# Optimization experiments

Hardware: AMD Instinct MI355X
Metric: run time of the kernel (lower is better)

Reference implementation:

```python
import jax, jax.numpy as jnp
import numpy as np
import math

Re = 0.15
DX = 1.0
UB = -1.0
NZ, NY, NX = 64, 256, 256
DT = 0.5
ITERATION = 2

def conv3(x, w, stride=1):
    return jax.lax.conv_general_dilated(x, w, (stride, stride, stride), 'VALID', dimension_numbers=('NCDHW', 'OIDHW', 'NCDHW'))

def pad1(x):
    return jnp.pad(x, ((0, 0), (0, 0), (1, 1), (1, 1), (1, 1)))

def bc_u(u):
    p = pad1(u)
    p = p.at[0, 0, :, :, 0].set(UB)
    p = p.at[0, 0, :, :, -1].set(UB)
    p = p.at[0, 0, :, 0, :].set(p[0, 0, :, 1, :])
    p = p.at[0, 0, :, -1, :].set(p[0, 0, :, -2, :])
    p = p.at[0, 0, 0, :, :].set(0.0)
    p = p.at[0, 0, -1, :, :].set(p[0, 0, -2, :, :])
    return p

def bc_v(v):
    # x faces, y faces, z-bottom are zero -> already satisfied by zero padding
    p = pad1(v)
    p = p.at[0, 0, -1, :, :].set(p[0, 0, -2, :, :])
    return p

def bc_w(w):
    # all six faces zero
    return pad1(w)

def bc_p(q):
    p = pad1(q)
    p = p.at[0, 0, :, :, 0].set(p[0, 0, :, :, 1])
    p = p.at[0, 0, :, :, -1].set(0.0)
    p = p.at[0, 0, :, 0, :].set(p[0, 0, :, 1, :])
    p = p.at[0, 0, :, -1, :].set(p[0, 0, :, -2, :])
    p = p.at[0, 0, 0, :, :].set(p[0, 0, 1, :, :])
    p = p.at[0, 0, -1, :, :].set(p[0, 0, -2, :, :])
    return p

def solid_body(u, v, w, sigma, dt):
    s = 1.0 / (1.0 + dt * sigma)
    return u * s, v * s, w * s

def prol(x):
    # nearest-neighbour upsample x2 in z, y, x
    return jnp.repeat(jnp.repeat(jnp.repeat(x, 2, axis=2), 2, axis=3), 2, axis=4)

def all_ads(uu, vv, ww, w1, w2, w3, w4):
    return (conv3(uu, w2), conv3(uu, w3), conv3(uu, w4),
            conv3(vv, w2), conv3(vv, w3), conv3(vv, w4),
            conv3(ww, w2), conv3(ww, w3), conv3(ww, w4),
            conv3(uu, w1), conv3(vv, w1), conv3(ww, w1))

def pg_vector(uu, vv, ww, u, v, w, k1, sigma, dt, w_diff, ads):
    ADx_u, ADy_u, ADz_u, ADx_v, ADy_v, ADz_v, ADx_w, ADy_w, ADz_w, AD2_u, AD2_v, AD2_w = ads
    speed = jnp.abs(u) * DX + jnp.abs(v) * DX + jnp.abs(w) * DX
    c = DX ** -3
    def kd(AD2, ax, ay, az):
        num = 0.1 * DX * jnp.abs((1.0 / 3.0) * c * speed * AD2)
        den = 0.001 + (jnp.abs(ax) * c + jnp.abs(ay) * c + jnp.abs(az) * c) / 3.0
        return num / den
    inv = 1.0 / (1.0 + dt * sigma)
    k_u = jnp.minimum(kd(AD2_u, ADx_u, ADy_u, ADz_u), k1) * inv
    k_v = jnp.minimum(kd(AD2_v, ADx_v, ADy_v, ADz_v), k1) * inv
    k_w = jnp.minimum(kd(AD2_w, ADx_w, ADy_w, ADz_w), k1) * inv
    # boundary_condition_k zeroes every halo face -> plain zero pad
    kuu, kvv, kww = pad1(k_u), pad1(k_v), pad1(k_w)
    k_x = 0.5 * (k_u * AD2_u + conv3(uu * kuu, w_diff) - u * conv3(kuu, w_diff))
    k_y = 0.5 * (k_v * AD2_v + conv3(vv * kvv, w_diff) - v * conv3(kvv, w_diff))
    k_z = 0.5 * (k_w * AD2_w + conv3(ww * kww, w_diff) - w * conv3(kww, w_diff))
    return k_x, k_y, k_z

def f_cycle_mg(uu, vv, ww, p, wA, w2, w3, w4, w_res, iteration, diag, dt, nlevel, ratio_x, ratio_y):
    b = -(conv3(uu, w2) + conv3(vv, w3) + conv3(ww, w4)) / dt
    w = jnp.zeros((1, 1, 2, 2 * ratio_y, 2 * ratio_x), b.dtype)
    r = b
    for _ in range(iteration):
        w = jnp.zeros((1, 1, 2, 2 * ratio_y, 2 * ratio_x), b.dtype)
        r = conv3(bc_p(p), wA) - b
        r_s = [r]
        for _ in range(1, nlevel - 1):
            r = conv3(r, w_res, stride=2)
            r_s.append(r)
        for i in reversed(range(1, nlevel - 1)):
            # boundary_condition_cw zeroes every halo face -> plain zero pad
            w = w - conv3(pad1(w), wA) / diag + r_s[i] / diag
            w = prol(w)
        p = p - w
        p = p - conv3(bc_p(p), wA) / diag + b / diag
    return p, w, r

def forward(values_u, values_v, values_w, values_p, k1, sigma, wA, w1, w2, w3, w4, w_res, dt, iteration):
    nz, ny, nx = values_u.shape[2], values_u.shape[3], values_u.shape[4]
    nlevel = int(math.log2(min(nx, ny, nz))) + 1
    ratio_x, ratio_y = nx // nz, ny // nz
    diag = wA[0, 0, 1, 1, 1]
    u, v, w = solid_body(values_u, values_v, values_w, sigma, dt)
    uu, vv, ww = bc_u(u), bc_v(v), bc_w(w)
    pp = bc_p(values_p)
    Gpx, Gpy, Gpz = conv3(pp, w2) * dt, conv3(pp, w3) * dt, conv3(pp, w4) * dt
    ads = all_ads(uu, vv, ww, w1, w2, w3, w4)
    k_x, k_y, k_z = pg_vector(uu, vv, ww, u, v, w, k1, sigma, dt, w1, ads)
    ADx_u, ADy_u, ADz_u, ADx_v, ADy_v, ADz_v, ADx_w, ADy_w, ADz_w, AD2_u, AD2_v, AD2_w = ads
    # predictor half step
    b_u = u + 0.5 * (Re * AD2_u * dt - u * ADx_u * dt - v * ADy_u * dt - w * ADz_u * dt) + 0.5 * k_x * dt - Gpx
    b_v = v + 0.5 * (Re * AD2_v * dt - u * ADx_v * dt - v * ADy_v * dt - w * ADz_v * dt) + 0.5 * k_y * dt - Gpy
    b_w = w + 0.5 * (Re * AD2_w * dt - u * ADx_w * dt - v * ADy_w * dt - w * ADz_w * dt) + 0.5 * k_z * dt - Gpz
    b_u, b_v, b_w = solid_body(b_u, b_v, b_w, sigma, dt)
    buu, bvv, bww = bc_u(b_u), bc_v(b_v), bc_w(b_w)
    ads = all_ads(buu, bvv, bww, w1, w2, w3, w4)
    k_x, k_y, k_z = pg_vector(buu, bvv, bww, b_u, b_v, b_w, k1, sigma, dt, w1, ads)
    ADx_u, ADy_u, ADz_u, ADx_v, ADy_v, ADz_v, ADx_w, ADy_w, ADz_w, AD2_u, AD2_v, AD2_w = ads
    # corrector full step
    u = u + Re * AD2_u * dt - b_u * ADx_u * dt - b_v * ADy_u * dt - b_w * ADz_u * dt + k_x * dt - Gpx
    v = v + Re * AD2_v * dt - b_u * ADx_v * dt - b_v * ADy_v * dt - b_w * ADz_v * dt + k_y * dt - Gpy
    w = w + Re * AD2_w * dt - b_u * ADx_w * dt - b_v * ADy_w * dt - b_w * ADz_w * dt + k_z * dt - Gpz
    u, v, w = solid_body(u, v, w, sigma, dt)
    uu, vv, ww = bc_u(u), bc_v(v), bc_w(w)
    p, w_mg, r = f_cycle_mg(uu, vv, ww, values_p, wA, w2, w3, w4, w_res, iteration, diag, dt, nlevel, ratio_x, ratio_y)
    # pressure-gradient velocity correction
    pp = bc_p(p)
    u = u - conv3(pp, w2) * dt
    v = v - conv3(pp, w3) * dt
    w = w - conv3(pp, w4) * dt
    u, v, w = solid_body(u, v, w, sigma, dt)
    return u, v, w, p, w_mg, r

def setup_inputs():
    key = jax.random.key(0)
    ks = jax.random.split(key, 4)
    f32 = jnp.float32
    shp = (1, 1, NZ, NY, NX)
    pshp = (1, 1, NZ + 2, NY + 2, NX + 2)
    lap = np.full((3, 3, 3), 1.0 / 26.0, np.float32)
    lap[1, 1, 1] = -1.0
    wA = jnp.asarray(lap.reshape(1, 1, 3, 3, 3))
    w1 = wA / (DX * DX)
    def cdiff(axis):
        k = np.zeros((3, 3, 3), np.float32)
        idx = [1, 1, 1]
        idx[axis] = 0
        k[tuple(idx)] = -0.5
        idx[axis] = 2
        k[tuple(idx)] = 0.5
        return jnp.asarray(k.reshape(1, 1, 3, 3, 3))
    w4, w3, w2 = cdiff(0), cdiff(1), cdiff(2)  # z, y, x advection stencils
    w_res = jnp.full((1, 1, 2, 2, 2), 0.125, f32)
    return dict(
        values_u=0.1 * jax.random.normal(ks[0], shp, f32),
        values_uu=jnp.zeros(pshp, f32),
        values_v=0.1 * jax.random.normal(ks[1], shp, f32),
        values_vv=jnp.zeros(pshp, f32),
        values_w=0.1 * jax.random.normal(ks[2], shp, f32),
        values_ww=jnp.zeros(pshp, f32),
        values_p=0.1 * jax.random.normal(ks[3], shp, f32),
        values_pp=jnp.zeros(pshp, f32),
        b_uu=jnp.zeros(pshp, f32), b_vv=jnp.zeros(pshp, f32), b_ww=jnp.zeros(pshp, f32),
        k1=2.0 * jnp.ones(shp, f32),
        k_uu=jnp.zeros(pshp, f32), k_vv=jnp.zeros(pshp, f32), k_ww=jnp.zeros(pshp, f32),
        sigma=jnp.zeros(shp, f32),
        wA=wA, w1=w1, w2=w2, w3=w3, w4=w4, w_res=w_res,
        dt=DT, iteration=ITERATION,
    )

def reference(values_u, values_uu, values_v, values_vv, values_w, values_ww, values_p, values_pp, b_uu, b_vv, b_ww, k1, k_uu, k_vv, k_ww, sigma, wA, w1, w2, w3, w4, w_res, dt, iteration):
    # padded scratch buffers (values_uu, ..., k_ww) are fully overwritten by the
    # boundary-condition routines, so the functional version rebuilds them via padding
    return forward(values_u, values_v, values_w, values_p, k1, sigma, wA, w1, w2, w3, w4, w_res, dt, iteration)
```

## Files before the change

kernel.cpp:

```cpp
#include <hip/hip_runtime.h>


#define RE_  0.15f
#define UB_  (-1.0f)
#define NZc  64
#define NYc  256
#define NXc  256
#define PZc  (NZc + 2)
#define PYc  (NYc + 2)
#define PXc  (NXc + 2)
#define Ncell  (NZc * NYc * NXc)
#define PNcell (PZc * PYc * PXc)

#define TBX 32
#define TBY 8
#define TZS 16

__device__ __forceinline__ int PIDX(int z, int y, int x) { return (z * PYc + y) * PXc + x; }
__device__ __forceinline__ int IDX (int z, int y, int x) { return (z * NYc + y) * NXc + x; }


struct PS {
  float s, c, xm, xp, ym, yp;
};
__device__ __forceinline__ PS rdp(const float* __restrict__ b, int pz, int iy, int ix) {
  PS q; q.s = 0.f;
#pragma unroll
  for (int dy = 0; dy < 3; ++dy) {
    int base = PIDX(pz, iy + dy, ix);
#pragma unroll
    for (int dx = 0; dx < 3; ++dx) {
      float v = b[base + dx];
      q.s += v;
      if (dy == 1 && dx == 1) q.c  = v;
      if (dy == 1 && dx == 0) q.xm = v;
      if (dy == 1 && dx == 2) q.xp = v;
      if (dy == 0 && dx == 1) q.ym = v;
      if (dy == 2 && dx == 1) q.yp = v;
    }
  }
  return q;
}

struct PS2 {
  float sv, svk, sk, vc, vxm, vxp, vym, vyp, kc;
};
__device__ __forceinline__ PS2 rdp2(const float* __restrict__ V, const float* __restrict__ K,
                                    int pz, int iy, int ix) {
  PS2 q; q.sv = 0.f; q.svk = 0.f; q.sk = 0.f;
#pragma unroll
  for (int dy = 0; dy < 3; ++dy) {
    int base = PIDX(pz, iy + dy, ix);
#pragma unroll
    for (int dx = 0; dx < 3; ++dx) {
      float v = V[base + dx], k = K[base + dx];
      q.sv += v; q.svk += v * k; q.sk += k;
      if (dy == 1 && dx == 1) { q.vc = v; q.kc = k; }
      if (dy == 1 && dx == 0) q.vxm = v;
      if (dy == 1 && dx == 2) q.vxp = v;
      if (dy == 0 && dx == 1) q.vym = v;
      if (dy == 2 && dx == 1) q.vyp = v;
    }
  }
  return q;
}

struct PR { float s, c; };
__device__ __forceinline__ PR rdpr(const float* __restrict__ b, int pz, int iy, int ix) {
  PR q; q.s = 0.f;
#pragma unroll
  for (int dy = 0; dy < 3; ++dy) {
    int base = PIDX(pz, iy + dy, ix);
#pragma unroll
    for (int dx = 0; dx < 3; ++dx) {
      float v = b[base + dx];
      q.s += v;
      if (dy == 1 && dx == 1) q.c = v;
    }
  }
  return q;
}


__global__ void k_scale_interior(const float* __restrict__ u0, const float* __restrict__ v0,
                                 const float* __restrict__ w0, const float* __restrict__ sigma,
                                 const float* __restrict__ dtp,
                                 float* __restrict__ Au, float* __restrict__ Av, float* __restrict__ Aw) {
  int i = blockIdx.x * blockDim.x + threadIdx.x;
  if (i >= Ncell) return;
  int x = i % NXc; int t = i / NXc; int y = t % NYc; int z = t / NYc;
  float s = 1.0f / (1.0f + dtp[0] * sigma[i]);
  int pi = PIDX(z + 1, y + 1, x + 1);
  Au[pi] = u0[i] * s;
  Av[pi] = v0[i] * s;
  Aw[pi] = w0[i] * s;
}

__global__ void k_halo_uvw(float* __restrict__ Au, float* __restrict__ Av, float* __restrict__ Aw) {
  int i = blockIdx.x * blockDim.x + threadIdx.x;
  if (i >= PNcell) return;
  int x = i % PXc; int t = i / PXc; int y = t % PYc; int z = t / PYc;
  if (z >= 1 && z <= NZc && y >= 1 && y <= NYc && x >= 1 && x <= NXc) return;
  float vu;
  if (z == 0) {
    vu = 0.0f;
  } else {
    int zz = (z == PZc - 1) ? NZc : z;
    if (x == 0 || x == PXc - 1) {
      vu = UB_;
    } else {
      int yy = y < 1 ? 1 : (y > NYc ? NYc : y);
      vu = Au[PIDX(zz, yy, x)];
    }
  }
  Au[i] = vu;
  float vv;
  if (z == 0 || x == 0 || x == PXc - 1 || y == 0 || y == PYc - 1) {
    vv = 0.0f;
  } else {
    vv = Av[PIDX(NZc, y, x)];
  }
  Av[i] = vv;
  Aw[i] = 0.0f;
}

__global__ void k_pad_p_interior(const float* __restrict__ p, float* __restrict__ pp) {
  int i = blockIdx.x * blockDim.x + threadIdx.x;
  if (i >= Ncell) return;
  int x = i % NXc; int t = i / NXc; int y = t % NYc; int z = t / NYc;
  pp[PIDX(z + 1, y + 1, x + 1)] = p[i];
}

__global__ void k_halo_p(float* __restrict__ pp) {
  int i = blockIdx.x * blockDim.x + threadIdx.x;
  if (i >= PNcell) return;
  int x = i % PXc; int t = i / PXc; int y = t % PYc; int z = t / PYc;
  if (z >= 1 && z <= NZc && y >= 1 && y <= NYc && x >= 1 && x <= NXc) return;
  float v;
  if (x == PXc - 1) {
    v = 0.0f;
  } else {
    int zz = z < 1 ? 1 : (z > NZc ? NZc : z);
    int yy = y < 1 ? 1 : (y > NYc ? NYc : y);
    int xx = (x == 0) ? 1 : x;
    v = pp[PIDX(zz, yy, xx)];
  }
  pp[i] = v;
}

__global__ void k_zero_halo3(float* __restrict__ a, float* __restrict__ b, float* __restrict__ c) {
  int i = blockIdx.x * blockDim.x + threadIdx.x;
  if (i >= PNcell) return;
  int x = i % PXc; int t = i / PXc; int y = t % PYc; int z = t / PYc;
  if (z >= 1 && z <= NZc && y >= 1 && y <= NYc && x >= 1 && x <= NXc) return;
  a[i] = 0.f; b[i] = 0.f; c[i] = 0.f;
}

__global__ void k_grad_p(const float* __restrict__ pp, const float* __restrict__ wx,
                         const float* __restrict__ wy, const float* __restrict__ wz,
                         const float* __restrict__ dtp,
                         float* __restrict__ gx, float* __restrict__ gy, float* __restrict__ gz) {
  int i = blockIdx.x * blockDim.x + threadIdx.x;
  if (i >= Ncell) return;
  int x = i % NXc; int t = i / NXc; int y = t % NYc; int z = t / NYc;
  float dt = dtp[0];
  gx[i] = (wx[12] * pp[PIDX(z + 1, y + 1, x)] + wx[14] * pp[PIDX(z + 1, y + 1, x + 2)]) * dt;
  gy[i] = (wy[10] * pp[PIDX(z + 1, y, x + 1)] + wy[16] * pp[PIDX(z + 1, y + 2, x + 1)]) * dt;
  gz[i] = (wz[4] * pp[PIDX(z, y + 1, x + 1)] + wz[22] * pp[PIDX(z + 2, y + 1, x + 1)]) * dt;
}

__global__ void k_div(const float* __restrict__ Au, const float* __restrict__ Av,
                      const float* __restrict__ Aw, const float* __restrict__ wx,
                      const float* __restrict__ wy, const float* __restrict__ wz,
                      const float* __restrict__ dtp, float* __restrict__ b) {
  int i = blockIdx.x * blockDim.x + threadIdx.x;
  if (i >= Ncell) return;
  int x = i % NXc; int t = i / NXc; int y = t % NYc; int z = t / NYc;
  float dx = wx[12] * Au[PIDX(z + 1, y + 1, x)] + wx[14] * Au[PIDX(z + 1, y + 1, x + 2)];
  float dy = wy[10] * Av[PIDX(z + 1, y, x + 1)] + wy[16] * Av[PIDX(z + 1, y + 2, x + 1)];
  float dz = wz[4] * Aw[PIDX(z, y + 1, x + 1)] + wz[22] * Aw[PIDX(z + 2, y + 1, x + 1)];
  b[i] = -(dx + dy + dz) / dtp[0];
}

__global__ void k_copy(const float* __restrict__ s, float* __restrict__ d, int n) {
  int i = blockIdx.x * blockDim.x + threadIdx.x;
  if (i < n) d[i] = s[i];
}

__global__ void k_restrict(const float* __restrict__ in, float* __restrict__ out,
                           int onz, int ony, int onx, const float* __restrict__ wres) {
  int i = blockIdx.x * blockDim.x + threadIdx.x;
  int tot = onz * ony * onx;
  if (i >= tot) return;
  int X = i % onx; int t = i / onx; int Y = t % ony; int Z = t / ony;
  int iny = ony * 2, inx = onx * 2;
  float s = 0.f;
#pragma unroll
  for (int dz = 0; dz < 2; ++dz)
#pragma unroll
    for (int dy = 0; dy < 2; ++dy)
#pragma unroll
      for (int dx = 0; dx < 2; ++dx)
        s += wres[(dz * 2 + dy) * 2 + dx] * in[((2 * Z + dz) * iny + 2 * Y + dy) * inx + 2 * X + dx];
  out[i] = s;
}

__global__ void k_up(const float* __restrict__ win, const float* __restrict__ r,
                     float* __restrict__ wout, int nz, int ny, int nx,
                     const float* __restrict__ wA, int first) {
  int i = blockIdx.x * blockDim.x + threadIdx.x;
  int tot = nz * ny * nx;
  if (i >= tot) return;
  int X = i % nx; int t = i / nx; int Y = t % ny; int Z = t / ny;
  float diag = wA[13];
  float val;
  if (first) {
    val = r[i] / diag;
  } else {
    float lap = 0.f;
#pragma unroll
    for (int dz = 0; dz < 3; ++dz)
#pragma unroll
      for (int dy = 0; dy < 3; ++dy)
#pragma unroll
        for (int dx = 0; dx < 3; ++dx) {
          int zz = Z + dz - 1, yy = Y + dy - 1, xx = X + dx - 1;
          if (zz >= 0 && zz < nz && yy >= 0 && yy < ny && xx >= 0 && xx < nx)
            lap += wA[(dz * 3 + dy) * 3 + dx] * win[(zz * ny + yy) * nx + xx];
        }
    val = win[i] - lap / diag + r[i] / diag;
  }
  int ony = 2 * ny, onx = 2 * nx;
#pragma unroll
  for (int dz = 0; dz < 2; ++dz)
#pragma unroll
    for (int dy = 0; dy < 2; ++dy)
#pragma unroll
      for (int dx = 0; dx < 2; ++dx)
        wout[((2 * Z + dz) * ony + (2 * Y + dy)) * onx + (2 * X + dx)] = val;
}

__global__ void k_sub_f(float* __restrict__ p, const float* __restrict__ w0,
                        float* __restrict__ pp) {
  int i = blockIdx.x * blockDim.x + threadIdx.x;
  if (i >= Ncell) return;
  int x = i % NXc; int t = i / NXc; int y = t % NYc; int z = t / NYc;
  float v = p[i] - w0[i];
  p[i] = v;
  pp[PIDX(z + 1, y + 1, x + 1)] = v;
}

__global__ void k_final(const float* __restrict__ Au, const float* __restrict__ Av,
                        const float* __restrict__ Aw, const float* __restrict__ pp,
                        const float* __restrict__ wx, const float* __restrict__ wy,
                        const float* __restrict__ wz, const float* __restrict__ sigma,
                        const float* __restrict__ dtp,
                        float* __restrict__ ou, float* __restrict__ ov, float* __restrict__ ow) {
  int i = blockIdx.x * blockDim.x + threadIdx.x;
  if (i >= Ncell) return;
  int x = i % NXc; int t = i / NXc; int y = t % NYc; int z = t / NYc;
  float dt = dtp[0];
  float inv = 1.0f / (1.0f + dt * sigma[i]);
  int pc = PIDX(z + 1, y + 1, x + 1);
  float dx = wx[12] * pp[PIDX(z + 1, y + 1, x)] + wx[14] * pp[PIDX(z + 1, y + 1, x + 2)];
  float dy = wy[10] * pp[PIDX(z + 1, y, x + 1)] + wy[16] * pp[PIDX(z + 1, y + 2, x + 1)];
  float dz = wz[4] * pp[PIDX(z, y + 1, x + 1)] + wz[22] * pp[PIDX(z + 2, y + 1, x + 1)];
  ou[i] = (Au[pc] - dx * dt) * inv;
  ov[i] = (Av[pc] - dy * dt) * inv;
  ow[i] = (Aw[pc] - dz * dt) * inv;
}


__global__ __launch_bounds__(256) void k_compute_k_t(
    const float* __restrict__ Au, const float* __restrict__ Av, const float* __restrict__ Aw,
    const float* __restrict__ k1, const float* __restrict__ sigma, const float* __restrict__ dtp,
    const float* __restrict__ w1, const float* __restrict__ wx, const float* __restrict__ wy,
    const float* __restrict__ wz,
    float* __restrict__ Ku, float* __restrict__ Kv, float* __restrict__ Kw) {
  int ix = blockIdx.x * TBX + threadIdx.x;
  int iy = blockIdx.y * TBY + threadIdx.y;
  int z0 = blockIdx.z * TZS;
  float dt = dtp[0];
  float wo = w1[0], wcd = w1[13] - wo;
  float cxm = wx[12], cxp = wx[14], cym = wy[10], cyp = wy[16], czm = wz[4], czp = wz[22];
  const float third = 1.0f / 3.0f;

  PS u0 = rdp(Au, z0, iy, ix), u1 = rdp(Au, z0 + 1, iy, ix);
  PS v0 = rdp(Av, z0, iy, ix), v1 = rdp(Av, z0 + 1, iy, ix);
  PS q0 = rdp(Aw, z0, iy, ix), q1 = rdp(Aw, z0 + 1, iy, ix);

  for (int iz = z0; iz < z0 + TZS; ++iz) {
    PS u2 = rdp(Au, iz + 2, iy, ix);
    PS v2 = rdp(Av, iz + 2, iy, ix);
    PS q2 = rdp(Aw, iz + 2, iy, ix);
    int ci = IDX(iz, iy, ix);
    float inv = 1.0f / (1.0f + dt * sigma[ci]);
    float k1v = k1[ci];
    float speed = fabsf(u1.c) + fabsf(v1.c) + fabsf(q1.c);
    int pc = PIDX(iz + 1, iy + 1, ix + 1);

    {
      float ad2 = wo * (u0.s + u1.s + u2.s) + wcd * u1.c;
      float ax = cxm * u1.xm + cxp * u1.xp;
      float ay = cym * u1.ym + cyp * u1.yp;
      float az = czm * u0.c + czp * u2.c;
      float num = 0.1f * fabsf(third * speed * ad2);
      float den = 0.001f + (fabsf(ax) + fabsf(ay) + fabsf(az)) * third;
      Ku[pc] = fminf(num / den, k1v) * inv;
    }
    {
      float ad2 = wo * (v0.s + v1.s + v2.s) + wcd * v1.c;
      float ax = cxm * v1.xm + cxp * v1.xp;
      float ay = cym * v1.ym + cyp * v1.yp;
      float az = czm * v0.c + czp * v2.c;
      float num = 0.1f * fabsf(third * speed * ad2);
      float den = 0.001f + (fabsf(ax) + fabsf(ay) + fabsf(az)) * third;
      Kv[pc] = fminf(num / den, k1v) * inv;
    }
    {
      float ad2 = wo * (q0.s + q1.s + q2.s) + wcd * q1.c;
      float ax = cxm * q1.xm + cxp * q1.xp;
      float ay = cym * q1.ym + cyp * q1.yp;
      float az = czm * q0.c + czp * q2.c;
      float num = 0.1f * fabsf(third * speed * ad2);
      float den = 0.001f + (fabsf(ax) + fabsf(ay) + fabsf(az)) * third;
      Kw[pc] = fminf(num / den, k1v) * inv;
    }
    u0 = u1; u1 = u2; v0 = v1; v1 = v2; q0 = q1; q1 = q2;
  }
}

__global__ __launch_bounds__(256) void k_compute_b_t(
    const float* __restrict__ Au, const float* __restrict__ Av, const float* __restrict__ Aw,
    const float* __restrict__ Ku, const float* __restrict__ Kv, const float* __restrict__ Kw,
    const float* __restrict__ gx, const float* __restrict__ gy, const float* __restrict__ gz,
    const float* __restrict__ sigma, const float* __restrict__ dtp,
    const float* __restrict__ w1, const float* __restrict__ wx, const float* __restrict__ wy,
    const float* __restrict__ wz,
    float* __restrict__ Bu, float* __restrict__ Bv, float* __restrict__ Bw) {
  int ix = blockIdx.x * TBX + threadIdx.x;
  int iy = blockIdx.y * TBY + threadIdx.y;
  int z0 = blockIdx.z * TZS;
  float dt = dtp[0];
  float wo = w1[0], wcd = w1[13] - wo;
  float cxm = wx[12], cxp = wx[14], cym = wy[10], cyp = wy[16], czm = wz[4], czp = wz[22];

  PS2 U0 = rdp2(Au, Ku, z0, iy, ix), U1 = rdp2(Au, Ku, z0 + 1, iy, ix);
  PS2 V0 = rdp2(Av, Kv, z0, iy, ix), V1 = rdp2(Av, Kv, z0 + 1, iy, ix);
  PS2 W0 = rdp2(Aw, Kw, z0, iy, ix), W1 = rdp2(Aw, Kw, z0 + 1, iy, ix);

  for (int iz = z0; iz < z0 + TZS; ++iz) {
    PS2 U2 = rdp2(Au, Ku, iz + 2, iy, ix);
    PS2 V2 = rdp2(Av, Kv, iz + 2, iy, ix);
    PS2 W2 = rdp2(Aw, Kw, iz + 2, iy, ix);
    int ci = IDX(iz, iy, ix);
    float inv = 1.0f / (1.0f + dt * sigma[ci]);
    float uc = U1.vc, vc = V1.vc, wc = W1.vc;
    int pc = PIDX(iz + 1, iy + 1, ix + 1);

    float ad2 = wo * (U0.sv + U1.sv + U2.sv) + wcd * uc;
    float suk = wo * (U0.svk + U1.svk + U2.svk) + wcd * uc * U1.kc;
    float sk  = wo * (U0.sk + U1.sk + U2.sk) + wcd * U1.kc;
    float kx = 0.5f * (U1.kc * ad2 + suk - uc * sk);
    float ax = cxm * U1.vxm + cxp * U1.vxp;
    float ay = cym * U1.vym + cyp * U1.vyp;
    float az = czm * U0.vc + czp * U2.vc;
    float bu = uc + 0.5f * dt * (RE_ * ad2 - uc * ax - vc * ay - wc * az) + 0.5f * kx * dt - gx[ci];

    ad2 = wo * (V0.sv + V1.sv + V2.sv) + wcd * vc;
    suk = wo * (V0.svk + V1.svk + V2.svk) + wcd * vc * V1.kc;
    sk  = wo * (V0.sk + V1.sk + V2.sk) + wcd * V1.kc;
    kx = 0.5f * (V1.kc * ad2 + suk - vc * sk);
    ax = cxm * V1.vxm + cxp * V1.vxp;
    ay = cym * V1.vym + cyp * V1.vyp;
    az = czm * V0.vc + czp * V2.vc;
    float bv = vc + 0.5f * dt * (RE_ * ad2 - uc * ax - vc * ay - wc * az) + 0.5f * kx * dt - gy[ci];

    ad2 = wo * (W0.sv + W1.sv + W2.sv) + wcd * wc;
    suk = wo * (W0.svk + W1.svk + W2.svk) + wcd * wc * W1.kc;
    sk  = wo * (W0.sk + W1.sk + W2.sk) + wcd * W1.kc;
    kx = 0.5f * (W1.kc * ad2 + suk - wc * sk);
    ax = cxm * W1.vxm + cxp * W1.vxp;
    ay = cym * W1.vym + cyp * W1.vyp;
    az = czm * W0.vc + czp * W2.vc;
    float bw = wc + 0.5f * dt * (RE_ * ad2 - uc * ax - vc * ay - wc * az) + 0.5f * kx * dt - gz[ci];

    Bu[pc] = bu * inv;
    Bv[pc] = bv * inv;
    Bw[pc] = bw * inv;
    U0 = U1; U1 = U2; V0 = V1; V1 = V2; W0 = W1; W1 = W2;
  }
}

__global__ __launch_bounds__(256) void k_corrector_t(
    float* __restrict__ Au, float* __restrict__ Av, float* __restrict__ Aw,
    const float* __restrict__ Bu, const float* __restrict__ Bv, const float* __restrict__ Bw,
    const float* __restrict__ Ku, const float* __restrict__ Kv, const float* __restrict__ Kw,
    const float* __restrict__ gx, const float* __restrict__ gy, const float* __restrict__ gz,
    const float* __restrict__ sigma, const float* __restrict__ dtp,
    const float* __restrict__ w1, const float* __restrict__ wx, const float* __restrict__ wy,
    const float* __restrict__ wz) {
  int ix = blockIdx.x * TBX + threadIdx.x;
  int iy = blockIdx.y * TBY + threadIdx.y;
  int z0 = blockIdx.z * TZS;
  float dt = dtp[0];
  float wo = w1[0], wcd = w1[13] - wo;
  float cxm = wx[12], cxp = wx[14], cym = wy[10], cyp = wy[16], czm = wz[4], czp = wz[22];

  PS2 U0 = rdp2(Bu, Ku, z0, iy, ix), U1 = rdp2(Bu, Ku, z0 + 1, iy, ix);
  PS2 V0 = rdp2(Bv, Kv, z0, iy, ix), V1 = rdp2(Bv, Kv, z0 + 1, iy, ix);
  PS2 W0 = rdp2(Bw, Kw, z0, iy, ix), W1 = rdp2(Bw, Kw, z0 + 1, iy, ix);

  for (int iz = z0; iz < z0 + TZS; ++iz) {
    PS2 U2 = rdp2(Bu, Ku, iz + 2, iy, ix);
    PS2 V2 = rdp2(Bv, Kv, iz + 2, iy, ix);
    PS2 W2 = rdp2(Bw, Kw, iz + 2, iy, ix);
    int ci = IDX(iz, iy, ix);
    float inv = 1.0f / (1.0f + dt * sigma[ci]);
    float buc = U1.vc, bvc = V1.vc, bwc = W1.vc;
    int pc = PIDX(iz + 1, iy + 1, ix + 1);

    float ad2 = wo * (U0.sv + U1.sv + U2.sv) + wcd * buc;
    float suk = wo * (U0.svk + U1.svk + U2.svk) + wcd * buc * U1.kc;
    float sk  = wo * (U0.sk + U1.sk + U2.sk) + wcd * U1.kc;
    float kx = 0.5f * (U1.kc * ad2 + suk - buc * sk);
    float ax = cxm * U1.vxm + cxp * U1.vxp;
    float ay = cym * U1.vym + cyp * U1.vyp;
    float az = czm * U0.vc + czp * U2.vc;
    float un = Au[pc] + RE_ * ad2 * dt - buc * ax * dt - bvc * ay * dt - bwc * az * dt + kx * dt - gx[ci];

    ad2 = wo * (V0.sv + V1.sv + V2.sv) + wcd * bvc;
    suk = wo * (V0.svk + V1.svk + V2.svk) + wcd * bvc * V1.kc;
    sk  = wo * (V0.sk + V1.sk + V2.sk) + wcd * V1.kc;
    kx = 0.5f * (V1.kc * ad2 + suk - bvc * sk);
    ax = cxm * V1.vxm + cxp * V1.vxp;
    ay = cym * V1.vym + cyp * V1.vyp;
    az = czm * V0.vc + czp * V2.vc;
    float vn = Av[pc] + RE_ * ad2 * dt - buc * ax * dt - bvc * ay * dt - bwc * az * dt + kx * dt - gy[ci];

    ad2 = wo * (W0.sv + W1.sv + W2.sv) + wcd * bwc;
    suk = wo * (W0.svk + W1.svk + W2.svk) + wcd * bwc * W1.kc;
    sk  = wo * (W0.sk + W1.sk + W2.sk) + wcd * W1.kc;
    kx = 0.5f * (W1.kc * ad2 + suk - bwc * sk);
    ax = cxm * W1.vxm + cxp * W1.vxp;
    ay = cym * W1.vym + cyp * W1.vyp;
    az = czm * W0.vc + czp * W2.vc;
    float wn = Aw[pc] + RE_ * ad2 * dt - buc * ax * dt - bvc * ay * dt - bwc * az * dt + kx * dt - gz[ci];

    Au[pc] = un * inv;
    Av[pc] = vn * inv;
    Aw[pc] = wn * inv;
    U0 = U1; U1 = U2; V0 = V1; V1 = V2; W0 = W1; W1 = W2;
  }
}

__global__ __launch_bounds__(256) void k_residual_t(
    const float* __restrict__ pp, const float* __restrict__ wA,
    const float* __restrict__ b, float* __restrict__ r0) {
  int ix = blockIdx.x * TBX + threadIdx.x;
  int iy = blockIdx.y * TBY + threadIdx.y;
  int z0 = blockIdx.z * TZS;
  float wo = wA[0], wcd = wA[13] - wo;
  PR p0 = rdpr(pp, z0, iy, ix), p1 = rdpr(pp, z0 + 1, iy, ix);
  for (int iz = z0; iz < z0 + TZS; ++iz) {
    PR p2 = rdpr(pp, iz + 2, iy, ix);
    int ci = IDX(iz, iy, ix);
    r0[ci] = wo * (p0.s + p1.s + p2.s) + wcd * p1.c - b[ci];
    p0 = p1; p1 = p2;
  }
}

__global__ __launch_bounds__(256) void k_smooth_t(
    const float* __restrict__ pp, const float* __restrict__ wA,
    const float* __restrict__ b, float* __restrict__ p, float* __restrict__ ppOut) {
  int ix = blockIdx.x * TBX + threadIdx.x;
  int iy = blockIdx.y * TBY + threadIdx.y;
  int z0 = blockIdx.z * TZS;
  float wo = wA[0], wcd = wA[13] - wo;
  float diag = wA[13];
  PR p0 = rdpr(pp, z0, iy, ix), p1 = rdpr(pp, z0 + 1, iy, ix);
  for (int iz = z0; iz < z0 + TZS; ++iz) {
    PR p2 = rdpr(pp, iz + 2, iy, ix);
    int ci = IDX(iz, iy, ix);
    float lap = wo * (p0.s + p1.s + p2.s) + wcd * p1.c;
    float v = p1.c - lap / diag + b[ci] / diag;
    p[ci] = v;
    ppOut[PIDX(iz + 1, iy + 1, ix + 1)] = v;
    p0 = p1; p1 = p2;
  }
}


extern "C" void kernel_launch(void* const* d_in, const int* in_sizes, int n_in,
                              void* d_out, int out_size, void* d_ws, size_t ws_size,
                              hipStream_t stream) {
  (void)in_sizes; (void)n_in; (void)out_size; (void)ws_size;

  const float* values_u = (const float*)d_in[0];
  const float* values_v = (const float*)d_in[2];
  const float* values_w = (const float*)d_in[4];
  const float* values_p = (const float*)d_in[6];
  const float* k1       = (const float*)d_in[11];
  const float* sigma    = (const float*)d_in[15];
  const float* wA       = (const float*)d_in[16];
  const float* w1       = (const float*)d_in[17];
  const float* w2       = (const float*)d_in[18];
  const float* w3       = (const float*)d_in[19];
  const float* w4       = (const float*)d_in[20];
  const float* wres     = (const float*)d_in[21];
  const float* dtp      = (const float*)d_in[22];
  const int ITER = 2;

  float* ws = (float*)d_ws;
  float* Au = ws + 0ll * PNcell;
  float* Av = ws + 1ll * PNcell;
  float* Aw = ws + 2ll * PNcell;
  float* Ku = ws + 3ll * PNcell;
  float* Kv = ws + 4ll * PNcell;
  float* Kw = ws + 5ll * PNcell;
  float* Bu = ws + 6ll * PNcell;
  float* Bv = ws + 7ll * PNcell;
  float* Bw = ws + 8ll * PNcell;
  float* ppA = ws + 9ll * PNcell;
  float* ppB = Ku;
  float* b_rhs = Bu;
  float* r0    = Bv;
  float* r1  = Bw;
  float* r2  = r1 + 524288;
  float* r3  = r2 + 65536;
  float* r4  = r3 + 8192;
  float* w1b = r4 + 1024;
  float* w2b = w1b + 524288;
  float* w3b = w2b + 65536;
  float* w4b = w3b + 8192;

  float* out_u   = (float*)d_out;
  float* out_v   = out_u + Ncell;
  float* out_w   = out_v + Ncell;
  float* out_p   = out_w + Ncell;
  float* out_wmg = out_p + Ncell;
  float* out_r   = out_wmg + Ncell;
  float* gx = out_u; float* gy = out_v; float* gz = out_w;

  const int B = 256;
  const int gN = (Ncell + B - 1) / B;
  const int gP = (PNcell + B - 1) / B;
  dim3 tblk(TBX, TBY, 1);
  dim3 tgrd(NXc / TBX, NYc / TBY, NZc / TZS);

  k_scale_interior<<<gN, B, 0, stream>>>(values_u, values_v, values_w, sigma, dtp, Au, Av, Aw);
  k_halo_uvw<<<gP, B, 0, stream>>>(Au, Av, Aw);
  k_pad_p_interior<<<gN, B, 0, stream>>>(values_p, ppA);
  k_halo_p<<<gP, B, 0, stream>>>(ppA);
  k_grad_p<<<gN, B, 0, stream>>>(ppA, w2, w3, w4, dtp, gx, gy, gz);

  k_zero_halo3<<<gP, B, 0, stream>>>(Ku, Kv, Kw);
  k_compute_k_t<<<tgrd, tblk, 0, stream>>>(Au, Av, Aw, k1, sigma, dtp, w1, w2, w3, w4, Ku, Kv, Kw);
  k_compute_b_t<<<tgrd, tblk, 0, stream>>>(Au, Av, Aw, Ku, Kv, Kw, gx, gy, gz, sigma, dtp,
                                           w1, w2, w3, w4, Bu, Bv, Bw);
  k_halo_uvw<<<gP, B, 0, stream>>>(Bu, Bv, Bw);

  k_compute_k_t<<<tgrd, tblk, 0, stream>>>(Bu, Bv, Bw, k1, sigma, dtp, w1, w2, w3, w4, Ku, Kv, Kw);
  k_corrector_t<<<tgrd, tblk, 0, stream>>>(Au, Av, Aw, Bu, Bv, Bw, Ku, Kv, Kw, gx, gy, gz,
                                           sigma, dtp, w1, w2, w3, w4);
  k_halo_uvw<<<gP, B, 0, stream>>>(Au, Av, Aw);

  k_div<<<gN, B, 0, stream>>>(Au, Av, Aw, w2, w3, w4, dtp, b_rhs);
  k_copy<<<gN, B, 0, stream>>>(values_p, out_p, Ncell);
  for (int it = 0; it < ITER; ++it) {
    k_residual_t<<<tgrd, tblk, 0, stream>>>(ppA, wA, b_rhs, r0);
    k_restrict<<<(524288 + B - 1) / B, B, 0, stream>>>(r0, r1, 32, 128, 128, wres);
    k_restrict<<<(65536 + B - 1) / B, B, 0, stream>>>(r1, r2, 16, 64, 64, wres);
    k_restrict<<<(8192 + B - 1) / B, B, 0, stream>>>(r2, r3, 8, 32, 32, wres);
    k_restrict<<<(1024 + B - 1) / B, B, 0, stream>>>(r3, r4, 4, 16, 16, wres);
    k_restrict<<<1, 128, 0, stream>>>(r4, out_r, 2, 8, 8, wres);
    k_up<<<1, 128, 0, stream>>>(nullptr, out_r, w4b, 2, 8, 8, wA, 1);
    k_up<<<(1024 + B - 1) / B, B, 0, stream>>>(w4b, r4, w3b, 4, 16, 16, wA, 0);
    k_up<<<(8192 + B - 1) / B, B, 0, stream>>>(w3b, r3, w2b, 8, 32, 32, wA, 0);
    k_up<<<(65536 + B - 1) / B, B, 0, stream>>>(w2b, r2, w1b, 16, 64, 64, wA, 0);
    k_up<<<(524288 + B - 1) / B, B, 0, stream>>>(w1b, r1, out_wmg, 32, 128, 128, wA, 0);
    k_sub_f<<<gN, B, 0, stream>>>(out_p, out_wmg, ppB);
    k_halo_p<<<gP, B, 0, stream>>>(ppB);
    k_smooth_t<<<tgrd, tblk, 0, stream>>>(ppB, wA, b_rhs, out_p, ppA);
    k_halo_p<<<gP, B, 0, stream>>>(ppA);
  }

  k_final<<<gN, B, 0, stream>>>(Au, Av, Aw, ppA, w2, w3, w4, sigma, dtp, out_u, out_v, out_w);
}
```

Baseline: 928.1 us.

## Stage stencil z-planes in double-buffered LDS tiles and launch halo kernels over halo cells only

The stencil kernels (k_compute_k_t, k_compute_b_t, k_corrector_t, residual, smooth) now cooperatively load each padded 34x10 z-plane into shared memory. The buffer is double-buffered, and the next plane is prefetched into registers while the current one is computed. This replaces the nine overlapping global loads per thread per plane, so repeated neighbour fetches come from LDS instead of the cache hierarchy. The halo kernels are also launched over only the boundary cell count rather than the full padded volume, which removes millions of idle threads that exited early. In exchange there is more shared memory per block and a barrier per z step, which could lower occupancy.

```diff
diff --git a/kernel.cpp b/kernel.cpp
--- a/kernel.cpp
+++ b/kernel.cpp
@@ -15,70 +15,420 @@
 #define TBX 32
 #define TBY 8
 #define TZS 16
+#define TLX 34
+#define TLY 10
+#define PL  340
+
+#define NHALO 198920
 
 __device__ __forceinline__ int PIDX(int z, int y, int x) { return (z * PYc + y) * PXc + x; }
 __device__ __forceinline__ int IDX (int z, int y, int x) { return (z * NYc + y) * NXc + x; }
 
-
-struct PS {
-  float s, c, xm, xp, ym, yp;
-};
-__device__ __forceinline__ PS rdp(const float* __restrict__ b, int pz, int iy, int ix) {
-  PS q; q.s = 0.f;
-#pragma unroll
-  for (int dy = 0; dy < 3; ++dy) {
-    int base = PIDX(pz, iy + dy, ix);
+struct F1 { float s, c, xm, xp, ym, yp; };
+__device__ __forceinline__ F1 rdf1(const float* sl, int ty, int tx) {
+  float t[3][3];
+#pragma unroll
+  for (int dy = 0; dy < 3; ++dy)
+#pragma unroll
+    for (int dx = 0; dx < 3; ++dx)
+      t[dy][dx] = sl[(ty + dy) * TLX + tx + dx];
+  F1 f;
+  f.s = t[0][0]+t[0][1]+t[0][2]+t[1][0]+t[1][1]+t[1][2]+t[2][0]+t[2][1]+t[2][2];
+  f.c = t[1][1]; f.xm = t[1][0]; f.xp = t[1][2]; f.ym = t[0][1]; f.yp = t[2][1];
+  return f;
+}
+
+struct F2 { float sv, svk, sk, vc, xm, xp, ym, yp, kc; };
+__device__ __forceinline__ F2 rdf2(const float* slv, const float* slk, int ty, int tx) {
+  float tv[3][3], tk[3][3];
+#pragma unroll
+  for (int dy = 0; dy < 3; ++dy)
 #pragma unroll
     for (int dx = 0; dx < 3; ++dx) {
-      float v = b[base + dx];
-      q.s += v;
-      if (dy == 1 && dx == 1) q.c  = v;
-      if (dy == 1 && dx == 0) q.xm = v;
-      if (dy == 1 && dx == 2) q.xp = v;
-      if (dy == 0 && dx == 1) q.ym = v;
-      if (dy == 2 && dx == 1) q.yp = v;
-    }
-  }
-  return q;
-}
-
-struct PS2 {
-  float sv, svk, sk, vc, vxm, vxp, vym, vyp, kc;
-};
-__device__ __forceinline__ PS2 rdp2(const float* __restrict__ V, const float* __restrict__ K,
-                                    int pz, int iy, int ix) {
-  PS2 q; q.sv = 0.f; q.svk = 0.f; q.sk = 0.f;
-#pragma unroll
-  for (int dy = 0; dy < 3; ++dy) {
-    int base = PIDX(pz, iy + dy, ix);
+      tv[dy][dx] = slv[(ty + dy) * TLX + tx + dx];
+      tk[dy][dx] = slk[(ty + dy) * TLX + tx + dx];
+    }
+  F2 f; f.sv = 0.f; f.svk = 0.f; f.sk = 0.f;
+#pragma unroll
+  for (int dy = 0; dy < 3; ++dy)
 #pragma unroll
     for (int dx = 0; dx < 3; ++dx) {
-      float v = V[base + dx], k = K[base + dx];
-      q.sv += v; q.svk += v * k; q.sk += k;
-      if (dy == 1 && dx == 1) { q.vc = v; q.kc = k; }
-      if (dy == 1 && dx == 0) q.vxm = v;
-      if (dy == 1 && dx == 2) q.vxp = v;
-      if (dy == 0 && dx == 1) q.vym = v;
-      if (dy == 2 && dx == 1) q.vyp = v;
-    }
-  }
-  return q;
-}
-
-struct PR { float s, c; };
-__device__ __forceinline__ PR rdpr(const float* __restrict__ b, int pz, int iy, int ix) {
-  PR q; q.s = 0.f;
-#pragma unroll
-  for (int dy = 0; dy < 3; ++dy) {
-    int base = PIDX(pz, iy + dy, ix);
-#pragma unroll
-    for (int dx = 0; dx < 3; ++dx) {
-      float v = b[base + dx];
-      q.s += v;
-      if (dy == 1 && dx == 1) q.c = v;
-    }
-  }
-  return q;
+      f.sv += tv[dy][dx]; f.svk += tv[dy][dx] * tk[dy][dx]; f.sk += tk[dy][dx];
+    }
+  f.vc = tv[1][1]; f.xm = tv[1][0]; f.xp = tv[1][2]; f.ym = tv[0][1]; f.yp = tv[2][1];
+  f.kc = tk[1][1];
+  return f;
+}
+
+struct R2s { float sv, svk, sk, vc; };
+struct R1s { float s, c; };
+
+#define SLOAD(G, pz, t0, t1) { \
+    t0 = (G)[PIDX((pz), by0 + q0r, bx0 + q0c)]; \
+    if (tid < PL - 256) t1 = (G)[PIDX((pz), by0 + q1r, bx0 + q1c)]; }
+#define SWRITE(L, slot, t0, t1) { \
+    (L)[(slot)][tid] = t0; \
+    if (tid < PL - 256) (L)[(slot)][256 + tid] = t1; }
+
+
+__global__ __launch_bounds__(256) void k_compute_k_t(
+    const float* __restrict__ Au, const float* __restrict__ Av, const float* __restrict__ Aw,
+    const float* __restrict__ k1, const float* __restrict__ sigma, const float* __restrict__ dtp,
+    const float* __restrict__ w1, const float* __restrict__ wx, const float* __restrict__ wy,
+    const float* __restrict__ wz,
+    float* __restrict__ Ku, float* __restrict__ Kv, float* __restrict__ Kw) {
+  __shared__ float Lu[2][PL], Lv[2][PL], Lw[2][PL];
+  const int tx = threadIdx.x, ty = threadIdx.y;
+  const int tid = ty * TBX + tx;
+  const int bx0 = blockIdx.x * TBX, by0 = blockIdx.y * TBY;
+  const int z0 = blockIdx.z * TZS;
+  const int q0r = tid / TLX, q0c = tid % TLX;
+  const int q1r = (256 + tid) / TLX, q1c = (256 + tid) % TLX;
+  const int ix = bx0 + tx, iy = by0 + ty;
+
+  float dt = dtp[0];
+  float wo = w1[0], wcd = w1[13] - wo;
+  float cxm = wx[12], cxp = wx[14], cym = wy[10], cyp = wy[16], czm = wz[4], czp = wz[22];
+  const float third = 1.0f / 3.0f;
+
+  float a0, a1, b0, b1, c0, c1;
+  SLOAD(Au, z0, a0, a1); SLOAD(Av, z0, b0, b1); SLOAD(Aw, z0, c0, c1);
+  SWRITE(Lu, 0, a0, a1); SWRITE(Lv, 0, b0, b1); SWRITE(Lw, 0, c0, c1);
+  __syncthreads();
+  F1 fu = rdf1(&Lu[0][0], ty, tx), fv = rdf1(&Lv[0][0], ty, tx), fw = rdf1(&Lw[0][0], ty, tx);
+  R1s p0u = {fu.s, fu.c}, p0v = {fv.s, fv.c}, p0w = {fw.s, fw.c};
+  SLOAD(Au, z0 + 1, a0, a1); SLOAD(Av, z0 + 1, b0, b1); SLOAD(Aw, z0 + 1, c0, c1);
+  SWRITE(Lu, 1, a0, a1); SWRITE(Lv, 1, b0, b1); SWRITE(Lw, 1, c0, c1);
+  __syncthreads();
+  F1 p1u = rdf1(&Lu[1][0], ty, tx), p1v = rdf1(&Lv[1][0], ty, tx), p1w = rdf1(&Lw[1][0], ty, tx);
+  SLOAD(Au, z0 + 2, a0, a1); SLOAD(Av, z0 + 2, b0, b1); SLOAD(Aw, z0 + 2, c0, c1);
+  SWRITE(Lu, 0, a0, a1); SWRITE(Lv, 0, b0, b1); SWRITE(Lw, 0, c0, c1);
+  __syncthreads();
+
+  for (int iz = z0; iz < z0 + TZS; ++iz) {
+    int rs = (iz - z0) & 1, wsl = rs ^ 1;
+    int pzn = iz + 3;
+    bool do_st = (pzn <= z0 + TZS + 1);
+    if (do_st) { SLOAD(Au, pzn, a0, a1); SLOAD(Av, pzn, b0, b1); SLOAD(Aw, pzn, c0, c1); }
+
+    int ci = IDX(iz, iy, ix);
+    float inv = 1.0f / (1.0f + dt * sigma[ci]);
+    float k1v = k1[ci];
+    float speed = fabsf(p1u.c) + fabsf(p1v.c) + fabsf(p1w.c);
+    int pc = PIDX(iz + 1, iy + 1, ix + 1);
+
+    fu = rdf1(&Lu[rs][0], ty, tx);
+    {
+      float ad2 = wo * (p0u.s + p1u.s + fu.s) + wcd * p1u.c;
+      float ax = cxm * p1u.xm + cxp * p1u.xp;
+      float ay = cym * p1u.ym + cyp * p1u.yp;
+      float az = czm * p0u.c + czp * fu.c;
+      float num = 0.1f * fabsf(third * speed * ad2);
+      float den = 0.001f + (fabsf(ax) + fabsf(ay) + fabsf(az)) * third;
+      Ku[pc] = fminf(num / den, k1v) * inv;
+    }
+    p0u.s = p1u.s; p0u.c = p1u.c; p1u = fu;
+
+    fv = rdf1(&Lv[rs][0], ty, tx);
+    {
+      float ad2 = wo * (p0v.s + p1v.s + fv.s) + wcd * p1v.c;
+      float ax = cxm * p1v.xm + cxp * p1v.xp;
+      float ay = cym * p1v.ym + cyp * p1v.yp;
+      float az = czm * p0v.c + czp * fv.c;
+      float num = 0.1f * fabsf(third * speed * ad2);
+      float den = 0.001f + (fabsf(ax) + fabsf(ay) + fabsf(az)) * third;
+      Kv[pc] = fminf(num / den, k1v) * inv;
+    }
+    p0v.s = p1v.s; p0v.c = p1v.c; p1v = fv;
+
+    fw = rdf1(&Lw[rs][0], ty, tx);
+    {
+      float ad2 = wo * (p0w.s + p1w.s + fw.s) + wcd * p1w.c;
+      float ax = cxm * p1w.xm + cxp * p1w.xp;
+      float ay = cym * p1w.ym + cyp * p1w.yp;
+      float az = czm * p0w.c + czp * fw.c;
+      float num = 0.1f * fabsf(third * speed * ad2);
+      float den = 0.001f + (fabsf(ax) + fabsf(ay) + fabsf(az)) * third;
+      Kw[pc] = fminf(num / den, k1v) * inv;
+    }
+    p0w.s = p1w.s; p0w.c = p1w.c; p1w = fw;
+
+    if (do_st) { SWRITE(Lu, wsl, a0, a1); SWRITE(Lv, wsl, b0, b1); SWRITE(Lw, wsl, c0, c1); }
+    __syncthreads();
+  }
+}
+
+__global__ __launch_bounds__(256) void k_compute_b_t(
+    const float* __restrict__ Au, const float* __restrict__ Av, const float* __restrict__ Aw,
+    const float* __restrict__ Ku, const float* __restrict__ Kv, const float* __restrict__ Kw,
+    const float* __restrict__ gx, const float* __restrict__ gy, const float* __restrict__ gz,
+    const float* __restrict__ sigma, const float* __restrict__ dtp,
+    const float* __restrict__ w1, const float* __restrict__ wx, const float* __restrict__ wy,
+    const float* __restrict__ wz,
+    float* __restrict__ Bu, float* __restrict__ Bv, float* __restrict__ Bw) {
+  __shared__ float Lu[2][PL], Lv[2][PL], Lw[2][PL], Lku[2][PL], Lkv[2][PL], Lkw[2][PL];
+  const int tx = threadIdx.x, ty = threadIdx.y;
+  const int tid = ty * TBX + tx;
+  const int bx0 = blockIdx.x * TBX, by0 = blockIdx.y * TBY;
+  const int z0 = blockIdx.z * TZS;
+  const int q0r = tid / TLX, q0c = tid % TLX;
+  const int q1r = (256 + tid) / TLX, q1c = (256 + tid) % TLX;
+  const int ix = bx0 + tx, iy = by0 + ty;
+
+  float dt = dtp[0];
+  float wo = w1[0], wcd = w1[13] - wo;
+  float cxm = wx[12], cxp = wx[14], cym = wy[10], cyp = wy[16], czm = wz[4], czp = wz[22];
+
+  float a0, a1, b0, b1, c0, c1, d0, d1, e0, e1, f0, f1;
+#define SLOAD6(pz) { SLOAD(Au, pz, a0, a1); SLOAD(Av, pz, b0, b1); SLOAD(Aw, pz, c0, c1); \
+                     SLOAD(Ku, pz, d0, d1); SLOAD(Kv, pz, e0, e1); SLOAD(Kw, pz, f0, f1); }
+#define SWRITE6(sl) { SWRITE(Lu, sl, a0, a1); SWRITE(Lv, sl, b0, b1); SWRITE(Lw, sl, c0, c1); \
+                      SWRITE(Lku, sl, d0, d1); SWRITE(Lkv, sl, e0, e1); SWRITE(Lkw, sl, f0, f1); }
+  SLOAD6(z0); SWRITE6(0); __syncthreads();
+  F2 fU = rdf2(&Lu[0][0], &Lku[0][0], ty, tx);
+  F2 fV = rdf2(&Lv[0][0], &Lkv[0][0], ty, tx);
+  F2 fW = rdf2(&Lw[0][0], &Lkw[0][0], ty, tx);
+  R2s p0u = {fU.sv, fU.svk, fU.sk, fU.vc};
+  R2s p0v = {fV.sv, fV.svk, fV.sk, fV.vc};
+  R2s p0w = {fW.sv, fW.svk, fW.sk, fW.vc};
+  SLOAD6(z0 + 1); SWRITE6(1); __syncthreads();
+  F2 p1u = rdf2(&Lu[1][0], &Lku[1][0], ty, tx);
+  F2 p1v = rdf2(&Lv[1][0], &Lkv[1][0], ty, tx);
+  F2 p1w = rdf2(&Lw[1][0], &Lkw[1][0], ty, tx);
+  SLOAD6(z0 + 2); SWRITE6(0); __syncthreads();
+
+  for (int iz = z0; iz < z0 + TZS; ++iz) {
+    int rs = (iz - z0) & 1, wsl = rs ^ 1;
+    int pzn = iz + 3;
+    bool do_st = (pzn <= z0 + TZS + 1);
+    if (do_st) SLOAD6(pzn);
+
+    int ci = IDX(iz, iy, ix);
+    float inv = 1.0f / (1.0f + dt * sigma[ci]);
+    float gxv = gx[ci], gyv = gy[ci], gzv = gz[ci];
+    float uc = p1u.vc, vc = p1v.vc, wc = p1w.vc;
+    int pc = PIDX(iz + 1, iy + 1, ix + 1);
+
+    fU = rdf2(&Lu[rs][0], &Lku[rs][0], ty, tx);
+    {
+      float ad2 = wo * (p0u.sv + p1u.sv + fU.sv) + wcd * uc;
+      float suk = wo * (p0u.svk + p1u.svk + fU.svk) + wcd * uc * p1u.kc;
+      float sk  = wo * (p0u.sk + p1u.sk + fU.sk) + wcd * p1u.kc;
+      float kx = 0.5f * (p1u.kc * ad2 + suk - uc * sk);
+      float ax = cxm * p1u.xm + cxp * p1u.xp;
+      float ay = cym * p1u.ym + cyp * p1u.yp;
+      float az = czm * p0u.vc + czp * fU.vc;
+      float bu = uc + 0.5f * dt * (RE_ * ad2 - uc * ax - vc * ay - wc * az) + 0.5f * kx * dt - gxv;
+      Bu[pc] = bu * inv;
+    }
+    p0u.sv = p1u.sv; p0u.svk = p1u.svk; p0u.sk = p1u.sk; p0u.vc = p1u.vc; p1u = fU;
+
+    fV = rdf2(&Lv[rs][0], &Lkv[rs][0], ty, tx);
+    {
+      float ad2 = wo * (p0v.sv + p1v.sv + fV.sv) + wcd * vc;
+      float suk = wo * (p0v.svk + p1v.svk + fV.svk) + wcd * vc * p1v.kc;
+      float sk  = wo * (p0v.sk + p1v.sk + fV.sk) + wcd * p1v.kc;
+      float kx = 0.5f * (p1v.kc * ad2 + suk - vc * sk);
+      float ax = cxm * p1v.xm + cxp * p1v.xp;
+      float ay = cym * p1v.ym + cyp * p1v.yp;
+      float az = czm * p0v.vc + czp * fV.vc;
+      float bv = vc + 0.5f * dt * (RE_ * ad2 - uc * ax - vc * ay - wc * az) + 0.5f * kx * dt - gyv;
+      Bv[pc] = bv * inv;
+    }
+    p0v.sv = p1v.sv; p0v.svk = p1v.svk; p0v.sk = p1v.sk; p0v.vc = p1v.vc; p1v = fV;
+
+    fW = rdf2(&Lw[rs][0], &Lkw[rs][0], ty, tx);
+    {
+      float ad2 = wo * (p0w.sv + p1w.sv + fW.sv) + wcd * wc;
+      float suk = wo * (p0w.svk + p1w.svk + fW.svk) + wcd * wc * p1w.kc;
+      float sk  = wo * (p0w.sk + p1w.sk + fW.sk) + wcd * p1w.kc;
+      float kx = 0.5f * (p1w.kc * ad2 + suk - wc * sk);
+      float ax = cxm * p1w.xm + cxp * p1w.xp;
+      float ay = cym * p1w.ym + cyp * p1w.yp;
+      float az = czm * p0w.vc + czp * fW.vc;
+      float bw = wc + 0.5f * dt * (RE_ * ad2 - uc * ax - vc * ay - wc * az) + 0.5f * kx * dt - gzv;
+      Bw[pc] = bw * inv;
+    }
+    p0w.sv = p1w.sv; p0w.svk = p1w.svk; p0w.sk = p1w.sk; p0w.vc = p1w.vc; p1w = fW;
+
+    if (do_st) SWRITE6(wsl);
+    __syncthreads();
+  }
+}
+
+__global__ __launch_bounds__(256) void k_corrector_t(
+    float* __restrict__ Au, float* __restrict__ Av, float* __restrict__ Aw,
+    const float* __restrict__ Bu, const float* __restrict__ Bv, const float* __restrict__ Bw,
+    const float* __restrict__ Ku, const float* __restrict__ Kv, const float* __restrict__ Kw,
+    const float* __restrict__ gx, const float* __restrict__ gy, const float* __restrict__ gz,
+    const float* __restrict__ sigma, const float* __restrict__ dtp,
+    const float* __restrict__ w1, const float* __restrict__ wx, const float* __restrict__ wy,
+    const float* __restrict__ wz) {
+  __shared__ float Lu[2][PL], Lv[2][PL], Lw[2][PL], Lku[2][PL], Lkv[2][PL], Lkw[2][PL];
+  const int tx = threadIdx.x, ty = threadIdx.y;
+  const int tid = ty * TBX + tx;
+  const int bx0 = blockIdx.x * TBX, by0 = blockIdx.y * TBY;
+  const int z0 = blockIdx.z * TZS;
+  const int q0r = tid / TLX, q0c = tid % TLX;
+  const int q1r = (256 + tid) / TLX, q1c = (256 + tid) % TLX;
+  const int ix = bx0 + tx, iy = by0 + ty;
+
+  float dt = dtp[0];
+  float wo = w1[0], wcd = w1[13] - wo;
+  float cxm = wx[12], cxp = wx[14], cym = wy[10], cyp = wy[16], czm = wz[4], czp = wz[22];
+
+  float a0, a1, b0, b1, c0, c1, d0, d1, e0, e1, f0, f1;
+#define SLOAD6B(pz) { SLOAD(Bu, pz, a0, a1); SLOAD(Bv, pz, b0, b1); SLOAD(Bw, pz, c0, c1); \
+                      SLOAD(Ku, pz, d0, d1); SLOAD(Kv, pz, e0, e1); SLOAD(Kw, pz, f0, f1); }
+  SLOAD6B(z0); SWRITE6(0); __syncthreads();
+  F2 fU = rdf2(&Lu[0][0], &Lku[0][0], ty, tx);
+  F2 fV = rdf2(&Lv[0][0], &Lkv[0][0], ty, tx);
+  F2 fW = rdf2(&Lw[0][0], &Lkw[0][0], ty, tx);
+  R2s p0u = {fU.sv, fU.svk, fU.sk, fU.vc};
+  R2s p0v = {fV.sv, fV.svk, fV.sk, fV.vc};
+  R2s p0w = {fW.sv, fW.svk, fW.sk, fW.vc};
+  SLOAD6B(z0 + 1); SWRITE6(1); __syncthreads();
+  F2 p1u = rdf2(&Lu[1][0], &Lku[1][0], ty, tx);
+  F2 p1v = rdf2(&Lv[1][0], &Lkv[1][0], ty, tx);
+  F2 p1w = rdf2(&Lw[1][0], &Lkw[1][0], ty, tx);
+  SLOAD6B(z0 + 2); SWRITE6(0); __syncthreads();
+
+  for (int iz = z0; iz < z0 + TZS; ++iz) {
+    int rs = (iz - z0) & 1, wsl = rs ^ 1;
+    int pzn = iz + 3;
+    bool do_st = (pzn <= z0 + TZS + 1);
+    if (do_st) SLOAD6B(pzn);
+
+    int ci = IDX(iz, iy, ix);
+    float inv = 1.0f / (1.0f + dt * sigma[ci]);
+    float gxv = gx[ci], gyv = gy[ci], gzv = gz[ci];
+    int pc = PIDX(iz + 1, iy + 1, ix + 1);
+    float auc = Au[pc], avc = Av[pc], awc = Aw[pc];
+    float buc = p1u.vc, bvc = p1v.vc, bwc = p1w.vc;
+
+    fU = rdf2(&Lu[rs][0], &Lku[rs][0], ty, tx);
+    float un;
+    {
+      float ad2 = wo * (p0u.sv + p1u.sv + fU.sv) + wcd * buc;
+      float suk = wo * (p0u.svk + p1u.svk + fU.svk) + wcd * buc * p1u.kc;
+      float sk  = wo * (p0u.sk + p1u.sk + fU.sk) + wcd * p1u.kc;
+      float kx = 0.5f * (p1u.kc * ad2 + suk - buc * sk);
+      float ax = cxm * p1u.xm + cxp * p1u.xp;
+      float ay = cym * p1u.ym + cyp * p1u.yp;
+      float az = czm * p0u.vc + czp * fU.vc;
+      un = auc + RE_ * ad2 * dt - buc * ax * dt - bvc * ay * dt - bwc * az * dt + kx * dt - gxv;
+    }
+    p0u.sv = p1u.sv; p0u.svk = p1u.svk; p0u.sk = p1u.sk; p0u.vc = p1u.vc; p1u = fU;
+
+    fV = rdf2(&Lv[rs][0], &Lkv[rs][0], ty, tx);
+    float vn;
+    {
+      float ad2 = wo * (p0v.sv + p1v.sv + fV.sv) + wcd * bvc;
+      float suk = wo * (p0v.svk + p1v.svk + fV.svk) + wcd * bvc * p1v.kc;
+      float sk  = wo * (p0v.sk + p1v.sk + fV.sk) + wcd * p1v.kc;
+      float kx = 0.5f * (p1v.kc * ad2 + suk - bvc * sk);
+      float ax = cxm * p1v.xm + cxp * p1v.xp;
+      float ay = cym * p1v.ym + cyp * p1v.yp;
+      float az = czm * p0v.vc + czp * fV.vc;
+      vn = avc + RE_ * ad2 * dt - buc * ax * dt - bvc * ay * dt - bwc * az * dt + kx * dt - gyv;
+    }
+    p0v.sv = p1v.sv; p0v.svk = p1v.svk; p0v.sk = p1v.sk; p0v.vc = p1v.vc; p1v = fV;
+
+    fW = rdf2(&Lw[rs][0], &Lkw[rs][0], ty, tx);
+    float wn;
+    {
+      float ad2 = wo * (p0w.sv + p1w.sv + fW.sv) + wcd * bwc;
+      float suk = wo * (p0w.svk + p1w.svk + fW.svk) + wcd * bwc * p1w.kc;
+      float sk  = wo * (p0w.sk + p1w.sk + fW.sk) + wcd * p1w.kc;
+      float kx = 0.5f * (p1w.kc * ad2 + suk - bwc * sk);
+      float ax = cxm * p1w.xm + cxp * p1w.xp;
+      float ay = cym * p1w.ym + cyp * p1w.yp;
+      float az = czm * p0w.vc + czp * fW.vc;
+      wn = awc + RE_ * ad2 * dt - buc * ax * dt - bvc * ay * dt - bwc * az * dt + kx * dt - gzv;
+    }
+    p0w.sv = p1w.sv; p0w.svk = p1w.svk; p0w.sk = p1w.sk; p0w.vc = p1w.vc; p1w = fW;
+
+    Au[pc] = un * inv;
+    Av[pc] = vn * inv;
+    Aw[pc] = wn * inv;
+
+    if (do_st) SWRITE6(wsl);
+    __syncthreads();
+  }
+}
+
+__global__ __launch_bounds__(256) void k_residual_t(
+    const float* __restrict__ pp, const float* __restrict__ wA,
+    const float* __restrict__ b, float* __restrict__ r0) {
+  __shared__ float Lp[2][PL];
+  const int tx = threadIdx.x, ty = threadIdx.y;
+  const int tid = ty * TBX + tx;
+  const int bx0 = blockIdx.x * TBX, by0 = blockIdx.y * TBY;
+  const int z0 = blockIdx.z * TZS;
+  const int q0r = tid / TLX, q0c = tid % TLX;
+  const int q1r = (256 + tid) / TLX, q1c = (256 + tid) % TLX;
+  const int ix = bx0 + tx, iy = by0 + ty;
+  float wo = wA[0], wcd = wA[13] - wo;
+
+  float a0, a1;
+  SLOAD(pp, z0, a0, a1); SWRITE(Lp, 0, a0, a1); __syncthreads();
+  F1 f = rdf1(&Lp[0][0], ty, tx);
+  R1s p0 = {f.s, f.c};
+  SLOAD(pp, z0 + 1, a0, a1); SWRITE(Lp, 1, a0, a1); __syncthreads();
+  F1 p1 = rdf1(&Lp[1][0], ty, tx);
+  SLOAD(pp, z0 + 2, a0, a1); SWRITE(Lp, 0, a0, a1); __syncthreads();
+
+  for (int iz = z0; iz < z0 + TZS; ++iz) {
+    int rs = (iz - z0) & 1, wsl = rs ^ 1;
+    int pzn = iz + 3;
+    bool do_st = (pzn <= z0 + TZS + 1);
+    if (do_st) SLOAD(pp, pzn, a0, a1);
+    int ci = IDX(iz, iy, ix);
+    f = rdf1(&Lp[rs][0], ty, tx);
+    r0[ci] = wo * (p0.s + p1.s + f.s) + wcd * p1.c - b[ci];
+    p0.s = p1.s; p0.c = p1.c; p1 = f;
+    if (do_st) SWRITE(Lp, wsl, a0, a1);
+    __syncthreads();
+  }
+}
+
+__global__ __launch_bounds__(256) void k_smooth_t(
+    const float* __restrict__ pp, const float* __restrict__ wA,
+    const float* __restrict__ b, float* __restrict__ p, float* __restrict__ ppOut) {
+  __shared__ float Lp[2][PL];
+  const int tx = threadIdx.x, ty = threadIdx.y;
+  const int tid = ty * TBX + tx;
+  const int bx0 = blockIdx.x * TBX, by0 = blockIdx.y * TBY;
+  const int z0 = blockIdx.z * TZS;
+  const int q0r = tid / TLX, q0c = tid % TLX;
+  const int q1r = (256 + tid) / TLX, q1c = (256 + tid) % TLX;
+  const int ix = bx0 + tx, iy = by0 + ty;
+  float wo = wA[0], wcd = wA[13] - wo;
+  float diag = wA[13];
+
+  float a0, a1;
+  SLOAD(pp, z0, a0, a1); SWRITE(Lp, 0, a0, a1); __syncthreads();
+  F1 f = rdf1(&Lp[0][0], ty, tx);
+  R1s p0 = {f.s, f.c};
+  SLOAD(pp, z0 + 1, a0, a1); SWRITE(Lp, 1, a0, a1); __syncthreads();
+  F1 p1 = rdf1(&Lp[1][0], ty, tx);
+  SLOAD(pp, z0 + 2, a0, a1); SWRITE(Lp, 0, a0, a1); __syncthreads();
+
+  for (int iz = z0; iz < z0 + TZS; ++iz) {
+    int rs = (iz - z0) & 1, wsl = rs ^ 1;
+    int pzn = iz + 3;
+    bool do_st = (pzn <= z0 + TZS + 1);
+    if (do_st) SLOAD(pp, pzn, a0, a1);
+    int ci = IDX(iz, iy, ix);
+    f = rdf1(&Lp[rs][0], ty, tx);
+    float lap = wo * (p0.s + p1.s + f.s) + wcd * p1.c;
+    float v = p1.c - lap / diag + b[ci] / diag;
+    p[ci] = v;
+    ppOut[PIDX(iz + 1, iy + 1, ix + 1)] = v;
+    p0.s = p1.s; p0.c = p1.c; p1 = f;
+    if (do_st) SWRITE(Lp, wsl, a0, a1);
+    __syncthreads();
+  }
 }
 
 
@@ -96,11 +446,34 @@
   Aw[pi] = w0[i] * s;
 }
 
+__device__ __forceinline__ void halo_decode(int t, int& z, int& y, int& x) {
+  if (t < 2 * PYc * PXc) {
+    z = (t >= PYc * PXc) ? PZc - 1 : 0;
+    int r = t % (PYc * PXc);
+    y = r / PXc; x = r % PXc;
+    return;
+  }
+  t -= 2 * PYc * PXc;
+  if (t < 2 * NZc * PXc) {
+    z = 1 + t / (2 * PXc);
+    int r = t % (2 * PXc);
+    y = (r >= PXc) ? PYc - 1 : 0;
+    x = r % PXc;
+    return;
+  }
+  t -= 2 * NZc * PXc;
+  z = 1 + t / (2 * NYc);
+  int r = t % (2 * NYc);
+  x = (r >= NYc) ? PXc - 1 : 0;
+  y = 1 + (r % NYc);
+}
+
 __global__ void k_halo_uvw(float* __restrict__ Au, float* __restrict__ Av, float* __restrict__ Aw) {
-  int i = blockIdx.x * blockDim.x + threadIdx.x;
-  if (i >= PNcell) return;
-  int x = i % PXc; int t = i / PXc; int y = t % PYc; int z = t / PYc;
-  if (z >= 1 && z <= NZc && y >= 1 && y <= NYc && x >= 1 && x <= NXc) return;
+  int t = blockIdx.x * blockDim.x + threadIdx.x;
+  if (t >= NHALO) return;
+  int z, y, x;
+  halo_decode(t, z, y, x);
+  int i = PIDX(z, y, x);
   float vu;
   if (z == 0) {
     vu = 0.0f;
@@ -124,18 +497,11 @@
   Aw[i] = 0.0f;
 }
 
-__global__ void k_pad_p_interior(const float* __restrict__ p, float* __restrict__ pp) {
-  int i = blockIdx.x * blockDim.x + threadIdx.x;
-  if (i >= Ncell) return;
-  int x = i % NXc; int t = i / NXc; int y = t % NYc; int z = t / NYc;
-  pp[PIDX(z + 1, y + 1, x + 1)] = p[i];
-}
-
 __global__ void k_halo_p(float* __restrict__ pp) {
-  int i = blockIdx.x * blockDim.x + threadIdx.x;
-  if (i >= PNcell) return;
-  int x = i % PXc; int t = i / PXc; int y = t % PYc; int z = t / PYc;
-  if (z >= 1 && z <= NZc && y >= 1 && y <= NYc && x >= 1 && x <= NXc) return;
+  int t = blockIdx.x * blockDim.x + threadIdx.x;
+  if (t >= NHALO) return;
+  int z, y, x;
+  halo_decode(t, z, y, x);
   float v;
   if (x == PXc - 1) {
     v = 0.0f;
@@ -145,15 +511,23 @@
     int xx = (x == 0) ? 1 : x;
     v = pp[PIDX(zz, yy, xx)];
   }
-  pp[i] = v;
+  pp[PIDX(z, y, x)] = v;
 }
 
 __global__ void k_zero_halo3(float* __restrict__ a, float* __restrict__ b, float* __restrict__ c) {
-  int i = blockIdx.x * blockDim.x + threadIdx.x;
-  if (i >= PNcell) return;
-  int x = i % PXc; int t = i / PXc; int y = t % PYc; int z = t / PYc;
-  if (z >= 1 && z <= NZc && y >= 1 && y <= NYc && x >= 1 && x <= NXc) return;
+  int t = blockIdx.x * blockDim.x + threadIdx.x;
+  if (t >= NHALO) return;
+  int z, y, x;
+  halo_decode(t, z, y, x);
+  int i = PIDX(z, y, x);
   a[i] = 0.f; b[i] = 0.f; c[i] = 0.f;
+}
+
+__global__ void k_pad_p_interior(const float* __restrict__ p, float* __restrict__ pp) {
+  int i = blockIdx.x * blockDim.x + threadIdx.x;
+  if (i >= Ncell) return;
+  int x = i % NXc; int t = i / NXc; int y = t % NYc; int z = t / NYc;
+  pp[PIDX(z + 1, y + 1, x + 1)] = p[i];
 }
 
 __global__ void k_grad_p(const float* __restrict__ pp, const float* __restrict__ wx,
@@ -268,226 +642,6 @@
   ou[i] = (Au[pc] - dx * dt) * inv;
   ov[i] = (Av[pc] - dy * dt) * inv;
   ow[i] = (Aw[pc] - dz * dt) * inv;
-}
-
-
-__global__ __launch_bounds__(256) void k_compute_k_t(
-    const float* __restrict__ Au, const float* __restrict__ Av, const float* __restrict__ Aw,
-    const float* __restrict__ k1, const float* __restrict__ sigma, const float* __restrict__ dtp,
-    const float* __restrict__ w1, const float* __restrict__ wx, const float* __restrict__ wy,
-    const float* __restrict__ wz,
-    float* __restrict__ Ku, float* __restrict__ Kv, float* __restrict__ Kw) {
-  int ix = blockIdx.x * TBX + threadIdx.x;
-  int iy = blockIdx.y * TBY + threadIdx.y;
-  int z0 = blockIdx.z * TZS;
-  float dt = dtp[0];
-  float wo = w1[0], wcd = w1[13] - wo;
-  float cxm = wx[12], cxp = wx[14], cym = wy[10], cyp = wy[16], czm = wz[4], czp = wz[22];
-  const float third = 1.0f / 3.0f;
-
-  PS u0 = rdp(Au, z0, iy, ix), u1 = rdp(Au, z0 + 1, iy, ix);
-  PS v0 = rdp(Av, z0, iy, ix), v1 = rdp(Av, z0 + 1, iy, ix);
-  PS q0 = rdp(Aw, z0, iy, ix), q1 = rdp(Aw, z0 + 1, iy, ix);
-
-  for (int iz = z0; iz < z0 + TZS; ++iz) {
-    PS u2 = rdp(Au, iz + 2, iy, ix);
-    PS v2 = rdp(Av, iz + 2, iy, ix);
-    PS q2 = rdp(Aw, iz + 2, iy, ix);
-    int ci = IDX(iz, iy, ix);
-    float inv = 1.0f / (1.0f + dt * sigma[ci]);
-    float k1v = k1[ci];
-    float speed = fabsf(u1.c) + fabsf(v1.c) + fabsf(q1.c);
-    int pc = PIDX(iz + 1, iy + 1, ix + 1);
-
-    {
-      float ad2 = wo * (u0.s + u1.s + u2.s) + wcd * u1.c;
-      float ax = cxm * u1.xm + cxp * u1.xp;
-      float ay = cym * u1.ym + cyp * u1.yp;
-      float az = czm * u0.c + czp * u2.c;
-      float num = 0.1f * fabsf(third * speed * ad2);
-      float den = 0.001f + (fabsf(ax) + fabsf(ay) + fabsf(az)) * third;
-      Ku[pc] = fminf(num / den, k1v) * inv;
-    }
-    {
-      float ad2 = wo * (v0.s + v1.s + v2.s) + wcd * v1.c;
-      float ax = cxm * v1.xm + cxp * v1.xp;
-      float ay = cym * v1.ym + cyp * v1.yp;
-      float az = czm * v0.c + czp * v2.c;
-      float num = 0.1f * fabsf(third * speed * ad2);
-      float den = 0.001f + (fabsf(ax) + fabsf(ay) + fabsf(az)) * third;
-      Kv[pc] = fminf(num / den, k1v) * inv;
-    }
-    {
-      float ad2 = wo * (q0.s + q1.s + q2.s) + wcd * q1.c;
-      float ax = cxm * q1.xm + cxp * q1.xp;
-      float ay = cym * q1.ym + cyp * q1.yp;
-      float az = czm * q0.c + czp * q2.c;
-      float num = 0.1f * fabsf(third * speed * ad2);
-      float den = 0.001f + (fabsf(ax) + fabsf(ay) + fabsf(az)) * third;
-      Kw[pc] = fminf(num / den, k1v) * inv;
-    }
-    u0 = u1; u1 = u2; v0 = v1; v1 = v2; q0 = q1; q1 = q2;
-  }
-}
-
-__global__ __launch_bounds__(256) void k_compute_b_t(
-    const float* __restrict__ Au, const float* __restrict__ Av, const float* __restrict__ Aw,
-    const float* __restrict__ Ku, const float* __restrict__ Kv, const float* __restrict__ Kw,
-    const float* __restrict__ gx, const float* __restrict__ gy, const float* __restrict__ gz,
-    const float* __restrict__ sigma, const float* __restrict__ dtp,
-    const float* __restrict__ w1, const float* __restrict__ wx, const float* __restrict__ wy,
-    const float* __restrict__ wz,
-    float* __restrict__ Bu, float* __restrict__ Bv, float* __restrict__ Bw) {
-  int ix = blockIdx.x * TBX + threadIdx.x;
-  int iy = blockIdx.y * TBY + threadIdx.y;
-  int z0 = blockIdx.z * TZS;
-  float dt = dtp[0];
-  float wo = w1[0], wcd = w1[13] - wo;
-  float cxm = wx[12], cxp = wx[14], cym = wy[10], cyp = wy[16], czm = wz[4], czp = wz[22];
-
-  PS2 U0 = rdp2(Au, Ku, z0, iy, ix), U1 = rdp2(Au, Ku, z0 + 1, iy, ix);
-  PS2 V0 = rdp2(Av, Kv, z0, iy, ix), V1 = rdp2(Av, Kv, z0 + 1, iy, ix);
-  PS2 W0 = rdp2(Aw, Kw, z0, iy, ix), W1 = rdp2(Aw, Kw, z0 + 1, iy, ix);
-
-  for (int iz = z0; iz < z0 + TZS; ++iz) {
-    PS2 U2 = rdp2(Au, Ku, iz + 2, iy, ix);
-    PS2 V2 = rdp2(Av, Kv, iz + 2, iy, ix);
-    PS2 W2 = rdp2(Aw, Kw, iz + 2, iy, ix);
-    int ci = IDX(iz, iy, ix);
-    float inv = 1.0f / (1.0f + dt * sigma[ci]);
-    float uc = U1.vc, vc = V1.vc, wc = W1.vc;
-    int pc = PIDX(iz + 1, iy + 1, ix + 1);
-
-    float ad2 = wo * (U0.sv + U1.sv + U2.sv) + wcd * uc;
-    float suk = wo * (U0.svk + U1.svk + U2.svk) + wcd * uc * U1.kc;
-    float sk  = wo * (U0.sk + U1.sk + U2.sk) + wcd * U1.kc;
-    float kx = 0.5f * (U1.kc * ad2 + suk - uc * sk);
-    float ax = cxm * U1.vxm + cxp * U1.vxp;
-    float ay = cym * U1.vym + cyp * U1.vyp;
-    float az = czm * U0.vc + czp * U2.vc;
-    float bu = uc + 0.5f * dt * (RE_ * ad2 - uc * ax - vc * ay - wc * az) + 0.5f * kx * dt - gx[ci];
-
-    ad2 = wo * (V0.sv + V1.sv + V2.sv) + wcd * vc;
-    suk = wo * (V0.svk + V1.svk + V2.svk) + wcd * vc * V1.kc;
-    sk  = wo * (V0.sk + V1.sk + V2.sk) + wcd * V1.kc;
-    kx = 0.5f * (V1.kc * ad2 + suk - vc * sk);
-    ax = cxm * V1.vxm + cxp * V1.vxp;
-    ay = cym * V1.vym + cyp * V1.vyp;
-    az = czm * V0.vc + czp * V2.vc;
-    float bv = vc + 0.5f * dt * (RE_ * ad2 - uc * ax - vc * ay - wc * az) + 0.5f * kx * dt - gy[ci];
-
-    ad2 = wo * (W0.sv + W1.sv + W2.sv) + wcd * wc;
-    suk = wo * (W0.svk + W1.svk + W2.svk) + wcd * wc * W1.kc;
-    sk  = wo * (W0.sk + W1.sk + W2.sk) + wcd * W1.kc;
-    kx = 0.5f * (W1.kc * ad2 + suk - wc * sk);
-    ax = cxm * W1.vxm + cxp * W1.vxp;
-    ay = cym * W1.vym + cyp * W1.vyp;
-    az = czm * W0.vc + czp * W2.vc;
-    float bw = wc + 0.5f * dt * (RE_ * ad2 - uc * ax - vc * ay - wc * az) + 0.5f * kx * dt - gz[ci];
-
-    Bu[pc] = bu * inv;
-    Bv[pc] = bv * inv;
-    Bw[pc] = bw * inv;
-    U0 = U1; U1 = U2; V0 = V1; V1 = V2; W0 = W1; W1 = W2;
-  }
-}
-
-__global__ __launch_bounds__(256) void k_corrector_t(
-    float* __restrict__ Au, float* __restrict__ Av, float* __restrict__ Aw,
-    const float* __restrict__ Bu, const float* __restrict__ Bv, const float* __restrict__ Bw,
-    const float* __restrict__ Ku, const float* __restrict__ Kv, const float* __restrict__ Kw,
-    const float* __restrict__ gx, const float* __restrict__ gy, const float* __restrict__ gz,
-    const float* __restrict__ sigma, const float* __restrict__ dtp,
-    const float* __restrict__ w1, const float* __restrict__ wx, const float* __restrict__ wy,
-    const float* __restrict__ wz) {
-  int ix = blockIdx.x * TBX + threadIdx.x;
-  int iy = blockIdx.y * TBY + threadIdx.y;
-  int z0 = blockIdx.z * TZS;
-  float dt = dtp[0];
-  float wo = w1[0], wcd = w1[13] - wo;
-  float cxm = wx[12], cxp = wx[14], cym = wy[10], cyp = wy[16], czm = wz[4], czp = wz[22];
-
-  PS2 U0 = rdp2(Bu, Ku, z0, iy, ix), U1 = rdp2(Bu, Ku, z0 + 1, iy, ix);
-  PS2 V0 = rdp2(Bv, Kv, z0, iy, ix), V1 = rdp2(Bv, Kv, z0 + 1, iy, ix);
-  PS2 W0 = rdp2(Bw, Kw, z0, iy, ix), W1 = rdp2(Bw, Kw, z0 + 1, iy, ix);
-
-  for (int iz = z0; iz < z0 + TZS; ++iz) {
-    PS2 U2 = rdp2(Bu, Ku, iz + 2, iy, ix);
-    PS2 V2 = rdp2(Bv, Kv, iz + 2, iy, ix);
-    PS2 W2 = rdp2(Bw, Kw, iz + 2, iy, ix);
-    int ci = IDX(iz, iy, ix);
-    float inv = 1.0f / (1.0f + dt * sigma[ci]);
-    float buc = U1.vc, bvc = V1.vc, bwc = W1.vc;
-    int pc = PIDX(iz + 1, iy + 1, ix + 1);
-
-    float ad2 = wo * (U0.sv + U1.sv + U2.sv) + wcd * buc;
-    float suk = wo * (U0.svk + U1.svk + U2.svk) + wcd * buc * U1.kc;
-    float sk  = wo * (U0.sk + U1.sk + U2.sk) + wcd * U1.kc;
-    float kx = 0.5f * (U1.kc * ad2 + suk - buc * sk);
-    float ax = cxm * U1.vxm + cxp * U1.vxp;
-    float ay = cym * U1.vym + cyp * U1.vyp;
-    float az = czm * U0.vc + czp * U2.vc;
-    float un = Au[pc] + RE_ * ad2 * dt - buc * ax * dt - bvc * ay * dt - bwc * az * dt + kx * dt - gx[ci];
-
-    ad2 = wo * (V0.sv + V1.sv + V2.sv) + wcd * bvc;
-    suk = wo * (V0.svk + V1.svk + V2.svk) + wcd * bvc * V1.kc;
-    sk  = wo * (V0.sk + V1.sk + V2.sk) + wcd * V1.kc;
-    kx = 0.5f * (V1.kc * ad2 + suk - bvc * sk);
-    ax = cxm * V1.vxm + cxp * V1.vxp;
-    ay = cym * V1.vym + cyp * V1.vyp;
-    az = czm * V0.vc + czp * V2.vc;
-    float vn = Av[pc] + RE_ * ad2 * dt - buc * ax * dt - bvc * ay * dt - bwc * az * dt + kx * dt - gy[ci];
-
-    ad2 = wo * (W0.sv + W1.sv + W2.sv) + wcd * bwc;
-    suk = wo * (W0.svk + W1.svk + W2.svk) + wcd * bwc * W1.kc;
-    sk  = wo * (W0.sk + W1.sk + W2.sk) + wcd * W1.kc;
-    kx = 0.5f * (W1.kc * ad2 + suk - bwc * sk);
-    ax = cxm * W1.vxm + cxp * W1.vxp;
-    ay = cym * W1.vym + cyp * W1.vyp;
-    az = czm * W0.vc + czp * W2.vc;
-    float wn = Aw[pc] + RE_ * ad2 * dt - buc * ax * dt - bvc * ay * dt - bwc * az * dt + kx * dt - gz[ci];
-
-    Au[pc] = un * inv;
-    Av[pc] = vn * inv;
-    Aw[pc] = wn * inv;
-    U0 = U1; U1 = U2; V0 = V1; V1 = V2; W0 = W1; W1 = W2;
-  }
-}
-
-__global__ __launch_bounds__(256) void k_residual_t(
-    const float* __restrict__ pp, const float* __restrict__ wA,
-    const float* __restrict__ b, float* __restrict__ r0) {
-  int ix = blockIdx.x * TBX + threadIdx.x;
-  int iy = blockIdx.y * TBY + threadIdx.y;
-  int z0 = blockIdx.z * TZS;
-  float wo = wA[0], wcd = wA[13] - wo;
-  PR p0 = rdpr(pp, z0, iy, ix), p1 = rdpr(pp, z0 + 1, iy, ix);
-  for (int iz = z0; iz < z0 + TZS; ++iz) {
-    PR p2 = rdpr(pp, iz + 2, iy, ix);
-    int ci = IDX(iz, iy, ix);
-    r0[ci] = wo * (p0.s + p1.s + p2.s) + wcd * p1.c - b[ci];
-    p0 = p1; p1 = p2;
-  }
-}
-
-__global__ __launch_bounds__(256) void k_smooth_t(
-    const float* __restrict__ pp, const float* __restrict__ wA,
-    const float* __restrict__ b, float* __restrict__ p, float* __restrict__ ppOut) {
-  int ix = blockIdx.x * TBX + threadIdx.x;
-  int iy = blockIdx.y * TBY + threadIdx.y;
-  int z0 = blockIdx.z * TZS;
-  float wo = wA[0], wcd = wA[13] - wo;
-  float diag = wA[13];
-  PR p0 = rdpr(pp, z0, iy, ix), p1 = rdpr(pp, z0 + 1, iy, ix);
-  for (int iz = z0; iz < z0 + TZS; ++iz) {
-    PR p2 = rdpr(pp, iz + 2, iy, ix);
-    int ci = IDX(iz, iy, ix);
-    float lap = wo * (p0.s + p1.s + p2.s) + wcd * p1.c;
-    float v = p1.c - lap / diag + b[ci] / diag;
-    p[ci] = v;
-    ppOut[PIDX(iz + 1, iy + 1, ix + 1)] = v;
-    p0 = p1; p1 = p2;
-  }
 }
 
 
@@ -544,26 +698,26 @@
 
   const int B = 256;
   const int gN = (Ncell + B - 1) / B;
-  const int gP = (PNcell + B - 1) / B;
+  const int gH = (NHALO + B - 1) / B;
   dim3 tblk(TBX, TBY, 1);
   dim3 tgrd(NXc / TBX, NYc / TBY, NZc / TZS);
 
   k_scale_interior<<<gN, B, 0, stream>>>(values_u, values_v, values_w, sigma, dtp, Au, Av, Aw);
-  k_halo_uvw<<<gP, B, 0, stream>>>(Au, Av, Aw);
+  k_halo_uvw<<<gH, B, 0, stream>>>(Au, Av, Aw);
   k_pad_p_interior<<<gN, B, 0, stream>>>(values_p, ppA);
-  k_halo_p<<<gP, B, 0, stream>>>(ppA);
+  k_halo_p<<<gH, B, 0, stream>>>(ppA);
   k_grad_p<<<gN, B, 0, stream>>>(ppA, w2, w3, w4, dtp, gx, gy, gz);
 
-  k_zero_halo3<<<gP, B, 0, stream>>>(Ku, Kv, Kw);
+  k_zero_halo3<<<gH, B, 0, stream>>>(Ku, Kv, Kw);
   k_compute_k_t<<<tgrd, tblk, 0, stream>>>(Au, Av, Aw, k1, sigma, dtp, w1, w2, w3, w4, Ku, Kv, Kw);
   k_compute_b_t<<<tgrd, tblk, 0, stream>>>(Au, Av, Aw, Ku, Kv, Kw, gx, gy, gz, sigma, dtp,
                                            w1, w2, w3, w4, Bu, Bv, Bw);
-  k_halo_uvw<<<gP, B, 0, stream>>>(Bu, Bv, Bw);
+  k_halo_uvw<<<gH, B, 0, stream>>>(Bu, Bv, Bw);
 
   k_compute_k_t<<<tgrd, tblk, 0, stream>>>(Bu, Bv, Bw, k1, sigma, dtp, w1, w2, w3, w4, Ku, Kv, Kw);
   k_corrector_t<<<tgrd, tblk, 0, stream>>>(Au, Av, Aw, Bu, Bv, Bw, Ku, Kv, Kw, gx, gy, gz,
                                            sigma, dtp, w1, w2, w3, w4);
-  k_halo_uvw<<<gP, B, 0, stream>>>(Au, Av, Aw);
+  k_halo_uvw<<<gH, B, 0, stream>>>(Au, Av, Aw);
 
   k_div<<<gN, B, 0, stream>>>(Au, Av, Aw, w2, w3, w4, dtp, b_rhs);
   k_copy<<<gN, B, 0, stream>>>(values_p, out_p, Ncell);
@@ -580,9 +734,9 @@
     k_up<<<(65536 + B - 1) / B, B, 0, stream>>>(w2b, r2, w1b, 16, 64, 64, wA, 0);
     k_up<<<(524288 + B - 1) / B, B, 0, stream>>>(w1b, r1, out_wmg, 32, 128, 128, wA, 0);
     k_sub_f<<<gN, B, 0, stream>>>(out_p, out_wmg, ppB);
-    k_halo_p<<<gP, B, 0, stream>>>(ppB);
+    k_halo_p<<<gH, B, 0, stream>>>(ppB);
     k_smooth_t<<<tgrd, tblk, 0, stream>>>(ppB, wA, b_rhs, out_p, ppA);
-    k_halo_p<<<gP, B, 0, stream>>>(ppA);
+    k_halo_p<<<gH, B, 0, stream>>>(ppA);
   }
 
   k_final<<<gN, B, 0, stream>>>(Au, Av, Aw, ppA, w2, w3, w4, sigma, dtp, out_u, out_v, out_w);
```

Result: faster. 806.9 us (-13.1%).
